# Kernel optimization log

Measured on AMD Instinct MI355X. Metric: run time of the kernel, lower is better.

## Reference

```python
import jax, jax.numpy as jnp
import numpy as np

H = 64        # index_n_heads
D = 128       # index_head_dim
R = 64        # rope_head_dim
TOPK = 512    # index_topk
FP8_MAX = 448.0
EPS = 1e-6
THETA = 10000.0


def setup_inputs() -> dict:
    key = jax.random.key(0)
    ks = jax.random.split(key, 6)
    T, DM, QL = 1536, 7168, 1536
    return {
        "hidden_states": jax.random.normal(ks[0], (T, DM), jnp.float32),
        "q_lora": jax.random.normal(ks[1], (T, QL), jnp.float32),
        "wq_b": jax.random.normal(ks[2], (QL, H * D), jnp.float32) / np.sqrt(QL),
        "wk": jax.random.normal(ks[3], (DM, D), jnp.float32) / np.sqrt(DM),
        "k_norm_w": jnp.ones((D,), jnp.float32),
        "k_norm_b": jnp.zeros((D,), jnp.float32),
        "weights_proj_w": jax.random.normal(ks[4], (DM, H), jnp.float32) / np.sqrt(DM),
        "positions": jnp.arange(T, dtype=jnp.int32),
    }


def _rope_neox(x, pos):
    # x: [T, ..., R]; pos: [T]. NEOX-style (half-split) rotary on the rope slice.
    half = R // 2
    inv = 1.0 / (THETA ** (jnp.arange(half, dtype=jnp.float32) / half))
    ang = pos.astype(jnp.float32)[:, None] * inv  # [T, half]
    cos, sin = jnp.cos(ang), jnp.sin(ang)
    while cos.ndim < x.ndim:
        cos, sin = cos[:, None, :], sin[:, None, :]
    x1, x2 = x[..., :half], x[..., half:]
    return jnp.concatenate([x1 * cos - x2 * sin, x2 * cos + x1 * sin], axis=-1)


def _fp8_quant(x):
    # per-row (last-dim) e4m3 quantization: value -> fp8 payload + fp32 scale
    scale = jnp.maximum(jnp.max(jnp.abs(x), axis=-1, keepdims=True) / FP8_MAX, 1e-12)
    xq = (x / scale).astype(jnp.float8_e4m3fn).astype(jnp.float32)
    return xq, scale


def reference(hidden_states, q_lora, wq_b, wk, k_norm_w, k_norm_b, weights_proj_w, positions):
    T = hidden_states.shape[0]
    softmax_scale = D ** (-0.5)
    weights_scale = H ** (-0.5)

    # projections
    q = (q_lora @ wq_b).reshape(T, H, D)          # wq_b
    k = hidden_states @ wk                        # wk

    # k_norm (LayerNorm)
    mu = jnp.mean(k, axis=-1, keepdims=True)
    var = jnp.mean((k - mu) ** 2, axis=-1, keepdims=True)
    k = (k - mu) * jax.lax.rsqrt(var + EPS) * k_norm_w + k_norm_b

    # RoPE on the first rope_head_dim dims of q and k
    q = jnp.concatenate([_rope_neox(q[..., :R], positions), q[..., R:]], axis=-1)
    k = jnp.concatenate([_rope_neox(k[..., :R], positions), k[..., R:]], axis=-1)

    # fp8 quantization (per token-head for q, per token for k)
    q_fp8, q_scale = _fp8_quant(q)   # [T,H,D], [T,H,1]
    k_fp8, k_scale = _fp8_quant(k)   # [T,D],   [T,1]

    # head-gate weights: weights_proj(x) * q_scale * softmax_scale * weights_scale
    gate = hidden_states @ weights_proj_w                      # [T,H]
    w = gate[..., None] * q_scale * (softmax_scale * weights_scale)  # [T,H,1]

    # index score: I[t,s] = sum_h w[t,h] * relu(q[t,h] . k[s]) * k_scale[s]
    qk = jnp.einsum('thd,sd->ths', q_fp8, k_fp8)               # [T,H,S]
    score = jnp.einsum('th,ths->ts', w[..., 0], jax.nn.relu(qk))
    score = score * k_scale[:, 0][None, :]

    # causal (ragged prefill) mask + topk block selection
    causal = positions[:, None] >= positions[None, :]
    score = jnp.where(causal, score, -jnp.inf)
    vals, idx = jax.lax.top_k(score, TOPK)
    idx = jnp.where(jnp.isfinite(vals), idx, -1)
    return idx, vals
```

## Files before the change

kernel.cpp:

```cpp
#include <hip/hip_runtime.h>
#include <hip/hip_bf16.h>
#include <math.h>

#define T_SZ 1536
#define DM_SZ 7168
#define QL_SZ 1536
#define H_SZ 64
#define D_SZ 128
#define ND 8192
#define TOPK_SZ 512
#define N2 192
#define SPLITK2 16

typedef float f32x4 __attribute__((ext_vector_type(4)));
typedef short s16x8 __attribute__((ext_vector_type(8)));
typedef unsigned long long u64;

static __device__ __forceinline__ unsigned char f32_to_e4m3(float x){
  unsigned int b = __float_as_uint(x);
  unsigned int s = (b >> 24) & 0x80u;
  float a = fabsf(x);
  if (a < 0.015625f){
    int m = (int)rintf(a * 512.0f);
    if (m == 8) return (unsigned char)(s | 0x08u);
    return (unsigned char)(s | (unsigned)m);
  }
  int e;
  float mant = frexpf(a, &e);
  int E = e - 1;
  int m = (int)rintf(mant * 16.0f) - 8;
  if (m == 8){ E += 1; m = 0; }
  if (E > 8 || (E == 8 && m > 6)) return (unsigned char)(s | 0x7Eu);
  return (unsigned char)(s | ((unsigned)(E + 7) << 3) | (unsigned)m);
}

static __device__ __forceinline__ unsigned short bf16_rne(float x){
  unsigned int u = __float_as_uint(x);
  return (unsigned short)((u + 0x7FFFu + ((u >> 16) & 1u)) >> 16);
}

typedef __attribute__((address_space(1))) const void gas_void;
typedef __attribute__((address_space(3))) void las_void;
static __device__ __forceinline__ void stage16(const void* g, void* l){
  __builtin_amdgcn_global_load_lds((gas_void*)g, (las_void*)l, 16, 0, 0);
}

__global__ void rope_table_k(const int* __restrict__ pos, float* __restrict__ cs){
  int i = blockIdx.x * blockDim.x + threadIdx.x;
  if (i >= T_SZ * 32) return;
  int t = i >> 5, j = i & 31;
  float inv = 1.0f / powf(10000.0f, (float)j * (1.0f / 32.0f));
  float ang = (float)pos[t] * inv;
  cs[t * 64 + j]      = cosf(ang);
  cs[t * 64 + 32 + j] = sinf(ang);
}

__global__ __launch_bounds__(256) void conv_split_k(const float* __restrict__ A,
                                                    unsigned short* __restrict__ hi,
                                                    unsigned short* __restrict__ lo,
                                                    int n4){
  int i = blockIdx.x * 256 + threadIdx.x;
  if (i >= n4) return;
  float4 v = *(const float4*)&A[(size_t)i * 4];
  float f[4] = {v.x, v.y, v.z, v.w};
  unsigned short hb[4], lb[4];
#pragma unroll
  for (int j = 0; j < 4; ++j){
    hb[j] = bf16_rne(f[j]);
    float hf = __uint_as_float((unsigned int)hb[j] << 16);
    lb[j] = bf16_rne(f[j] - hf);
  }
  ushort4 h, l;
  h.x = hb[0]; h.y = hb[1]; h.z = hb[2]; h.w = hb[3];
  l.x = lb[0]; l.y = lb[1]; l.z = lb[2]; l.w = lb[3];
  *(ushort4*)&hi[(size_t)i * 4] = h;
  *(ushort4*)&lo[(size_t)i * 4] = l;
}

__global__ __launch_bounds__(256) void convB_k(const float* __restrict__ B,
                                               unsigned short* __restrict__ bhi,
                                               unsigned short* __restrict__ blo){
  __shared__ float ld[32][33];
  const int n0 = blockIdx.x * 32, k0 = blockIdx.y * 32;
  const int t = threadIdx.x;
  const int r = t >> 3, c4 = (t & 7) * 4;
  float4 v = *(const float4*)&B[(size_t)(k0 + r) * ND + n0 + c4];
  ld[r][c4 + 0] = v.x; ld[r][c4 + 1] = v.y; ld[r][c4 + 2] = v.z; ld[r][c4 + 3] = v.w;
  __syncthreads();
  unsigned short hb[4], lb[4];
#pragma unroll
  for (int j = 0; j < 4; ++j){
    float x = ld[c4 + j][r];
    hb[j] = bf16_rne(x);
    float hf = __uint_as_float((unsigned int)hb[j] << 16);
    lb[j] = bf16_rne(x - hf);
  }
  ushort4 h, l;
  h.x = hb[0]; h.y = hb[1]; h.z = hb[2]; h.w = hb[3];
  l.x = lb[0]; l.y = lb[1]; l.z = lb[2]; l.w = lb[3];
  *(ushort4*)&bhi[(size_t)(n0 + r) * QL_SZ + k0 + c4] = h;
  *(ushort4*)&blo[(size_t)(n0 + r) * QL_SZ + k0 + c4] = l;
}

__global__ __launch_bounds__(256) void conv_w2_k(const float* __restrict__ wk,
                                                 const float* __restrict__ wp,
                                                 unsigned short* __restrict__ bhi,
                                                 unsigned short* __restrict__ blo){
  __shared__ float ld[32][33];
  const int n0 = blockIdx.x * 32, k0 = blockIdx.y * 32;
  const int t = threadIdx.x;
  const int r = t >> 3, c4 = (t & 7) * 4;
  float4 v;
  if (n0 < 128) v = *(const float4*)&wk[(size_t)(k0 + r) * 128 + n0 + c4];
  else          v = *(const float4*)&wp[(size_t)(k0 + r) * 64 + (n0 - 128) + c4];
  ld[r][c4 + 0] = v.x; ld[r][c4 + 1] = v.y; ld[r][c4 + 2] = v.z; ld[r][c4 + 3] = v.w;
  __syncthreads();
  unsigned short hb[4], lb[4];
#pragma unroll
  for (int j = 0; j < 4; ++j){
    float x = ld[c4 + j][r];
    hb[j] = bf16_rne(x);
    float hf = __uint_as_float((unsigned int)hb[j] << 16);
    lb[j] = bf16_rne(x - hf);
  }
  ushort4 h, l;
  h.x = hb[0]; h.y = hb[1]; h.z = hb[2]; h.w = hb[3];
  l.x = lb[0]; l.y = lb[1]; l.z = lb[2]; l.w = lb[3];
  *(ushort4*)&bhi[(size_t)(n0 + r) * DM_SZ + k0 + c4] = h;
  *(ushort4*)&blo[(size_t)(n0 + r) * DM_SZ + k0 + c4] = l;
}

__global__ __launch_bounds__(256) void gemm1_mfma_k(const unsigned short* __restrict__ Ahi,
                                                    const unsigned short* __restrict__ Alo,
                                                    const unsigned short* __restrict__ Bhi,
                                                    const unsigned short* __restrict__ Blo,
                                                    float* __restrict__ C){
  __shared__ unsigned short As [128 * 64];
  __shared__ unsigned short Bs0[128 * 64];
  __shared__ unsigned short Bs1[128 * 64];
  const int bid = blockIdx.x;
  const int lid = (bid & 7) * 96 + (bid >> 3);
  const int mt = lid % 12, nt = lid / 12;
  const int m0 = mt * 128, n0 = nt * 128;
  const int tid = threadIdx.x;
  const int w = tid >> 6, l = tid & 63;
  const int wr = w >> 1, wc = w & 1;
  const int lr = l & 15, lg = l >> 4;

  const int srow = w * 32 + (l >> 3);
  const int ssl  = (l & 7) ^ ((l >> 3) & 7);
  const size_t gA = (size_t)(m0 + srow) * QL_SZ + ssl * 8;
  const size_t gB = (size_t)(n0 + srow) * QL_SZ + ssl * 8;
  const int lbase = w * 2048;

  f32x4 acc[4][4];
#pragma unroll
  for (int i = 0; i < 4; ++i)
#pragma unroll
    for (int j = 0; j < 4; ++j) acc[i][j] = (f32x4){0.f, 0.f, 0.f, 0.f};

  const int amrow = wr * 64 + lr;
  const int bnrow = wc * 64 + lr;

  for (int k0 = 0; k0 < QL_SZ; k0 += 64){
#pragma unroll
    for (int i = 0; i < 4; ++i){
      size_t go = (size_t)i * 8 * QL_SZ + k0;
      stage16(Ahi + gA + go, As  + lbase + i * 512);
      stage16(Bhi + gB + go, Bs0 + lbase + i * 512);
      stage16(Blo + gB + go, Bs1 + lbase + i * 512);
    }
    __syncthreads();
#pragma unroll
    for (int kk = 0; kk < 2; ++kk){
      s16x8 af[4], b0[4], b1[4];
#pragma unroll
      for (int f = 0; f < 4; ++f){
        int ma = amrow + f * 16;
        int nb = bnrow + f * 16;
        int sa = ((kk * 4 + lg) ^ (ma & 7)) * 16;
        int sb = ((kk * 4 + lg) ^ (nb & 7)) * 16;
        af[f] = *(const s16x8*)((const char*)As  + ma * 128 + sa);
        b0[f] = *(const s16x8*)((const char*)Bs0 + nb * 128 + sb);
        b1[f] = *(const s16x8*)((const char*)Bs1 + nb * 128 + sb);
      }
#pragma unroll
      for (int fi = 0; fi < 4; ++fi)
#pragma unroll
        for (int fj = 0; fj < 4; ++fj)
          acc[fi][fj] = __builtin_amdgcn_mfma_f32_16x16x32_bf16(af[fi], b0[fj], acc[fi][fj], 0, 0, 0);
#pragma unroll
      for (int fi = 0; fi < 4; ++fi)
#pragma unroll
        for (int fj = 0; fj < 4; ++fj)
          acc[fi][fj] = __builtin_amdgcn_mfma_f32_16x16x32_bf16(af[fi], b1[fj], acc[fi][fj], 0, 0, 0);
    }
    __syncthreads();
#pragma unroll
    for (int i = 0; i < 4; ++i)
      stage16(Alo + gA + (size_t)i * 8 * QL_SZ + k0, As + lbase + i * 512);
    __syncthreads();
#pragma unroll
    for (int kk = 0; kk < 2; ++kk){
      s16x8 af[4], b0[4];
#pragma unroll
      for (int f = 0; f < 4; ++f){
        int ma = amrow + f * 16;
        int nb = bnrow + f * 16;
        af[f] = *(const s16x8*)((const char*)As  + ma * 128 + (((kk * 4 + lg) ^ (ma & 7)) * 16));
        b0[f] = *(const s16x8*)((const char*)Bs0 + nb * 128 + (((kk * 4 + lg) ^ (nb & 7)) * 16));
      }
#pragma unroll
      for (int fi = 0; fi < 4; ++fi)
#pragma unroll
        for (int fj = 0; fj < 4; ++fj)
          acc[fi][fj] = __builtin_amdgcn_mfma_f32_16x16x32_bf16(af[fi], b0[fj], acc[fi][fj], 0, 0, 0);
    }
    __syncthreads();
  }

#pragma unroll
  for (int fi = 0; fi < 4; ++fi){
    const int row = m0 + wr * 64 + fi * 16 + lg * 4;
#pragma unroll
    for (int fj = 0; fj < 4; ++fj){
      float* cp = C + (size_t)row * ND + n0 + wc * 64 + fj * 16 + lr;
      f32x4 d = acc[fi][fj];
      cp[0]              = d.x;
      cp[(size_t)ND]     = d.y;
      cp[(size_t)2 * ND] = d.z;
      cp[(size_t)3 * ND] = d.w;
    }
  }
}

__global__ __launch_bounds__(128) void gemm2_mfma_k(const unsigned short* __restrict__ Ahi,
                                                    const unsigned short* __restrict__ Alo,
                                                    const unsigned short* __restrict__ Bhi,
                                                    const unsigned short* __restrict__ Blo,
                                                    float* __restrict__ part){
  __shared__ unsigned short As [128 * 64];
  __shared__ unsigned short Bs0[64 * 64];
  __shared__ unsigned short Bs1[64 * 64];
  const int bid = blockIdx.x;
  const int lid = (bid & 7) * 72 + (bid >> 3);
  const int s   = lid / 36;
  const int rem = lid % 36;
  const int mt = rem / 3, nt = rem % 3;
  const int m0 = mt * 128, n0 = nt * 64;
  const int kbeg = s * (DM_SZ / SPLITK2);
  const int tid = threadIdx.x;
  const int w = tid >> 6, l = tid & 63;
  const int lr = l & 15, lg = l >> 4;

  const int srow = tid >> 3;
  const int ssl  = (tid & 7) ^ (srow & 7);
  const size_t gA = (size_t)(m0 + srow) * DM_SZ + ssl * 8;
  const size_t gB = (size_t)(n0 + srow) * DM_SZ + ssl * 8;
  const int lbase = w * 512;

  f32x4 acc[4][4];
#pragma unroll
  for (int i = 0; i < 4; ++i)
#pragma unroll
    for (int j = 0; j < 4; ++j) acc[i][j] = (f32x4){0.f, 0.f, 0.f, 0.f};

  const int amrow = w * 64 + lr;
  const int bnrow = lr;

  for (int k0 = kbeg; k0 < kbeg + DM_SZ / SPLITK2; k0 += 64){
#pragma unroll
    for (int i = 0; i < 8; ++i)
      stage16(Ahi + gA + (size_t)i * 16 * DM_SZ + k0, As + lbase + i * 1024);
#pragma unroll
    for (int i = 0; i < 4; ++i){
      stage16(Bhi + gB + (size_t)i * 16 * DM_SZ + k0, Bs0 + lbase + i * 1024);
      stage16(Blo + gB + (size_t)i * 16 * DM_SZ + k0, Bs1 + lbase + i * 1024);
    }
    __syncthreads();
#pragma unroll
    for (int kk = 0; kk < 2; ++kk){
      s16x8 af[4], b0[4], b1[4];
#pragma unroll
      for (int f = 0; f < 4; ++f){
        int ma = amrow + f * 16;
        int nb = bnrow + f * 16;
        int sa = ((kk * 4 + lg) ^ (ma & 7)) * 16;
        int sb = ((kk * 4 + lg) ^ (nb & 7)) * 16;
        af[f] = *(const s16x8*)((const char*)As  + ma * 128 + sa);
        b0[f] = *(const s16x8*)((const char*)Bs0 + nb * 128 + sb);
        b1[f] = *(const s16x8*)((const char*)Bs1 + nb * 128 + sb);
      }
#pragma unroll
      for (int fi = 0; fi < 4; ++fi)
#pragma unroll
        for (int fj = 0; fj < 4; ++fj)
          acc[fi][fj] = __builtin_amdgcn_mfma_f32_16x16x32_bf16(af[fi], b0[fj], acc[fi][fj], 0, 0, 0);
#pragma unroll
      for (int fi = 0; fi < 4; ++fi)
#pragma unroll
        for (int fj = 0; fj < 4; ++fj)
          acc[fi][fj] = __builtin_amdgcn_mfma_f32_16x16x32_bf16(af[fi], b1[fj], acc[fi][fj], 0, 0, 0);
    }
    __syncthreads();
#pragma unroll
    for (int i = 0; i < 8; ++i)
      stage16(Alo + gA + (size_t)i * 16 * DM_SZ + k0, As + lbase + i * 1024);
    __syncthreads();
#pragma unroll
    for (int kk = 0; kk < 2; ++kk){
      s16x8 af[4], b0[4];
#pragma unroll
      for (int f = 0; f < 4; ++f){
        int ma = amrow + f * 16;
        int nb = bnrow + f * 16;
        af[f] = *(const s16x8*)((const char*)As  + ma * 128 + (((kk * 4 + lg) ^ (ma & 7)) * 16));
        b0[f] = *(const s16x8*)((const char*)Bs0 + nb * 128 + (((kk * 4 + lg) ^ (nb & 7)) * 16));
      }
#pragma unroll
      for (int fi = 0; fi < 4; ++fi)
#pragma unroll
        for (int fj = 0; fj < 4; ++fj)
          acc[fi][fj] = __builtin_amdgcn_mfma_f32_16x16x32_bf16(af[fi], b0[fj], acc[fi][fj], 0, 0, 0);
    }
    __syncthreads();
  }

  float* p = part + (size_t)(s * 36 + mt * 3 + nt) * (128 * 64);
#pragma unroll
  for (int fi = 0; fi < 4; ++fi){
    const int row = w * 64 + fi * 16 + lg * 4;
#pragma unroll
    for (int fj = 0; fj < 4; ++fj){
      float* cp = p + (size_t)row * 64 + fj * 16 + lr;
      f32x4 d = acc[fi][fj];
      cp[  0] = d.x;
      cp[ 64] = d.y;
      cp[128] = d.z;
      cp[192] = d.w;
    }
  }
}

__global__ void gemm2_reduce2_k(const float* __restrict__ part,
                                float* __restrict__ kraw, float* __restrict__ gate){
  int e = blockIdx.x * 256 + threadIdx.x;
  if (e >= T_SZ * N2) return;
  int r = e / N2, c = e % N2;
  int mt = r >> 7, rl = r & 127;
  int nt = c >> 6, cl = c & 63;
  const float* pp = part + (size_t)(mt * 3 + nt) * (128 * 64) + rl * 64 + cl;
  float sum = 0.0f;
#pragma unroll
  for (int s = 0; s < SPLITK2; ++s) sum += pp[(size_t)s * 36 * 128 * 64];
  if (c < 128) kraw[r * 128 + c] = sum;
  else         gate[r * 64 + (c - 128)] = sum;
}

__global__ __launch_bounds__(256) void gemm1_k(const float* __restrict__ A,
                                               const float* __restrict__ B,
                                               float* __restrict__ C){
  __shared__ float As[8][132];
  __shared__ float Bs[8][132];
  const int tid = threadIdx.x;
  const int bm = blockIdx.y * 128, bn = blockIdx.x * 128;
  const int ty = tid >> 4, tx = tid & 15;
  const int arow = tid >> 1, ak = (tid & 1) * 4;
  const int brow = tid >> 5, bcol = (tid & 31) * 4;
  float acc[8][8];
#pragma unroll
  for (int i = 0; i < 8; i++)
#pragma unroll
    for (int j = 0; j < 8; j++) acc[i][j] = 0.0f;

  for (int k0 = 0; k0 < QL_SZ; k0 += 8){
    float4 av = *(const float4*)&A[(size_t)(bm + arow) * QL_SZ + k0 + ak];
    float4 bv = *(const float4*)&B[(size_t)(k0 + brow) * ND + bn + bcol];
    As[ak + 0][arow] = av.x; As[ak + 1][arow] = av.y;
    As[ak + 2][arow] = av.z; As[ak + 3][arow] = av.w;
    *(float4*)&Bs[brow][bcol] = bv;
    __syncthreads();
#pragma unroll
    for (int kk = 0; kk < 8; ++kk){
      float a[8], b[8];
      *(float4*)&a[0] = *(const float4*)&As[kk][ty * 8];
      *(float4*)&a[4] = *(const float4*)&As[kk][ty * 8 + 4];
      *(float4*)&b[0] = *(const float4*)&Bs[kk][tx * 8];
      *(float4*)&b[4] = *(const float4*)&Bs[kk][tx * 8 + 4];
#pragma unroll
      for (int i = 0; i < 8; i++)
#pragma unroll
        for (int j = 0; j < 8; j++) acc[i][j] += a[i] * b[j];
    }
    __syncthreads();
  }
#pragma unroll
  for (int i = 0; i < 8; i++)
#pragma unroll
    for (int j = 0; j < 8; j += 4){
      float4 o; o.x = acc[i][j]; o.y = acc[i][j+1]; o.z = acc[i][j+2]; o.w = acc[i][j+3];
      *(float4*)&C[(size_t)(bm + ty * 8 + i) * ND + bn + tx * 8 + j] = o;
    }
}

__global__ __launch_bounds__(256) void gemm2_partial_k(const float* __restrict__ hs,
                                                       const float* __restrict__ wk,
                                                       const float* __restrict__ wp,
                                                       float* __restrict__ part){
  __shared__ float As[32][33];
  __shared__ float Bs[32][196];
  const int tid = threadIdx.x;
  const int m0 = blockIdx.x * 32;
  const int ks = blockIdx.y;
  const int kbeg = ks * (DM_SZ / 8), kend = kbeg + DM_SZ / 8;
  const int arow = tid >> 3, ak4 = (tid & 7) * 4;
  const int r2 = (tid >> 4) * 2, cg = (tid & 15) * 12;
  float acc[2][12];
#pragma unroll
  for (int i = 0; i < 2; i++)
#pragma unroll
    for (int j = 0; j < 12; j++) acc[i][j] = 0.0f;

  for (int k0 = kbeg; k0 < kend; k0 += 32){
    float4 av = *(const float4*)&hs[(size_t)(m0 + arow) * DM_SZ + k0 + ak4];
    As[ak4 + 0][arow] = av.x; As[ak4 + 1][arow] = av.y;
    As[ak4 + 2][arow] = av.z; As[ak4 + 3][arow] = av.w;
#pragma unroll
    for (int i = 0; i < 6; ++i){
      int fi = tid + i * 256;
      int row = fi / 48, c4 = fi % 48;
      float4 bv;
      if (c4 < 32) bv = *(const float4*)&wk[(size_t)(k0 + row) * 128 + c4 * 4];
      else         bv = *(const float4*)&wp[(size_t)(k0 + row) * 64 + (c4 - 32) * 4];
      *(float4*)&Bs[row][c4 * 4] = bv;
    }
    __syncthreads();
#pragma unroll
    for (int kk = 0; kk < 32; ++kk){
      float a0 = As[kk][r2], a1 = As[kk][r2 + 1];
      float b[12];
      *(float4*)&b[0] = *(const float4*)&Bs[kk][cg];
      *(float4*)&b[4] = *(const float4*)&Bs[kk][cg + 4];
      *(float4*)&b[8] = *(const float4*)&Bs[kk][cg + 8];
#pragma unroll
      for (int j = 0; j < 12; j++){ acc[0][j] += a0 * b[j]; acc[1][j] += a1 * b[j]; }
    }
    __syncthreads();
  }
  float* p = part + (size_t)(ks * 48 + blockIdx.x) * 32 * 192;
#pragma unroll
  for (int i = 0; i < 2; i++)
#pragma unroll
    for (int j = 0; j < 12; j += 4){
      float4 o; o.x = acc[i][j]; o.y = acc[i][j+1]; o.z = acc[i][j+2]; o.w = acc[i][j+3];
      *(float4*)&p[(r2 + i) * 192 + cg + j] = o;
    }
}

__global__ void gemm2_reduce_k(const float* __restrict__ part,
                               float* __restrict__ kraw, float* __restrict__ gate){
  int e = blockIdx.x * 256 + threadIdx.x;
  if (e >= T_SZ * 192) return;
  int r = e / 192, c = e % 192;
  int mt = r >> 5, rl = r & 31;
  float s = 0.0f;
  for (int ks = 0; ks < 8; ++ks)
    s += part[((size_t)(ks * 48 + mt) * 32 + rl) * 192 + c];
  if (c < 128) kraw[r * 128 + c] = s;
  else         gate[r * 64 + (c - 128)] = s;
}

__global__ __launch_bounds__(128) void k_post_k(const float* __restrict__ kraw,
                                                const float* __restrict__ knw,
                                                const float* __restrict__ knb,
                                                const float* __restrict__ cs,
                                                unsigned char* __restrict__ kf8,
                                                float* __restrict__ kscale){
  const int t = blockIdx.x, d = threadIdx.x;
  __shared__ float sh[128];
  __shared__ float red[2];
  float x = kraw[t * 128 + d];
  float v = x;
#pragma unroll
  for (int o = 32; o > 0; o >>= 1) v += __shfl_xor(v, o, 64);
  if ((d & 63) == 0) red[d >> 6] = v;
  __syncthreads();
  float mu = (red[0] + red[1]) / 128.0f;
  float dx = x - mu;
  v = dx * dx;
  __syncthreads();
#pragma unroll
  for (int o = 32; o > 0; o >>= 1) v += __shfl_xor(v, o, 64);
  if ((d & 63) == 0) red[d >> 6] = v;
  __syncthreads();
  float var = (red[0] + red[1]) / 128.0f;
  float nv = dx * (1.0f / sqrtf(var + 1e-6f)) * knw[d] + knb[d];
  sh[d] = nv;
  __syncthreads();
  float outv;
  const float* ct = cs + t * 64;
  if (d < 32)        outv = nv * ct[d] - sh[d + 32] * ct[32 + d];
  else if (d < 64){ int j = d - 32; outv = nv * ct[j] + sh[j] * ct[32 + j]; }
  else               outv = nv;
  v = fabsf(outv);
  __syncthreads();
#pragma unroll
  for (int o = 32; o > 0; o >>= 1) v = fmaxf(v, __shfl_xor(v, o, 64));
  if ((d & 63) == 0) red[d >> 6] = v;
  __syncthreads();
  float amax = fmaxf(red[0], red[1]);
  float scale = fmaxf(amax / 448.0f, 1e-12f);
  kf8[t * 128 + d] = f32_to_e4m3(outv / scale);
  if (d == 0) kscale[t] = scale;
}

__global__ __launch_bounds__(256) void q_post2_k(const float* __restrict__ q,
                                                 const float* __restrict__ gate,
                                                 const float* __restrict__ cs,
                                                 unsigned char* __restrict__ qf8,
                                                 float* __restrict__ wbuf){
  const int t = blockIdx.x, tid = threadIdx.x;
  const int h = tid >> 2, g = tid & 3;
  __shared__ float sh[64 * 132];
  const float* qrow = q + (size_t)t * 8192;
#pragma unroll
  for (int i = 0; i < 8; ++i){
    int e4 = tid + i * 256;
    int hh = e4 >> 5, dd = (e4 & 31) * 4;
    float4 v = *(const float4*)&qrow[(size_t)e4 * 4];
    float* dst = &sh[hh * 132 + dd];
    dst[0] = v.x; dst[1] = v.y; dst[2] = v.z; dst[3] = v.w;
  }
  __syncthreads();
  const float* ct = cs + t * 64;
  const float* hq = sh + h * 132;
  float x[32];
#pragma unroll
  for (int j = 0; j < 32; ++j) x[j] = hq[g + 4 * j];
  float vals[32];
  float am = 0.0f;
#pragma unroll
  for (int j = 0; j < 8; ++j){
    int d = g + 4 * j;
    float c = ct[d], s = ct[32 + d];
    float lo = x[j] * c - x[j + 8] * s;
    float hi = x[j + 8] * c + x[j] * s;
    vals[j] = lo; vals[j + 8] = hi;
    am = fmaxf(am, fmaxf(fabsf(lo), fabsf(hi)));
  }
#pragma unroll
  for (int j = 16; j < 32; ++j){ vals[j] = x[j]; am = fmaxf(am, fabsf(x[j])); }
  am = fmaxf(am, __shfl_xor(am, 1, 64));
  am = fmaxf(am, __shfl_xor(am, 2, 64));
  float scale = fmaxf(am / 448.0f, 1e-12f);
  unsigned char* qp = qf8 + (size_t)t * 8192 + h * 128 + g;
#pragma unroll
  for (int j = 0; j < 32; ++j) qp[4 * j] = f32_to_e4m3(vals[j] / scale);
  if (g == 0) wbuf[t * 64 + h] = gate[t * 64 + h] * scale * 0.011048543456039806f;
}

__global__ __launch_bounds__(256) void score_mfma_k(const unsigned char* __restrict__ qf8,
                                                    const unsigned char* __restrict__ kf8,
                                                    const float* __restrict__ wbuf,
                                                    const float* __restrict__ kscale,
                                                    float* __restrict__ score){
  const int bid = blockIdx.x;
  const int p = bid >> 1;
  const int h0 = (bid & 1) * 32;
  int bt = (int)((sqrtf(8.0f * (float)p + 1.0f) - 1.0f) * 0.5f);
  while ((bt + 1) * (bt + 2) / 2 <= p) ++bt;
  while (bt * (bt + 1) / 2 > p) --bt;
  const int bs = p - bt * (bt + 1) / 2;
  const int t0 = bt * 64, s0 = bs * 64;
  const int tid = threadIdx.x;
  const int w  = tid >> 6;
  const int l  = tid & 63;
  const int lr = l & 15;
  const int lg = l >> 4;

  __shared__ float wl[64][68];
#pragma unroll
  for (int i = 0; i < 4; i++){
    int fi = tid + i * 256;
    int row = fi >> 4, c4 = (fi & 15) * 4;
    *(float4*)&wl[row][c4] = *(const float4*)&wbuf[(t0 + row) * 64 + c4];
  }

  u64 b00,b01,b02,b03, b10,b11,b12,b13, b20,b21,b22,b23, b30,b31,b32,b33;
  {
    const unsigned char* kb = kf8 + (size_t)s0 * 128 + 8 * lg;
    const unsigned char* k0r = kb + (size_t)(lr     ) * 128;
    const unsigned char* k1r = kb + (size_t)(lr + 16) * 128;
    const unsigned char* k2r = kb + (size_t)(lr + 32) * 128;
    const unsigned char* k3r = kb + (size_t)(lr + 48) * 128;
    b00=*(const u64*)(k0r+0);  b01=*(const u64*)(k0r+32); b02=*(const u64*)(k0r+64); b03=*(const u64*)(k0r+96);
    b10=*(const u64*)(k1r+0);  b11=*(const u64*)(k1r+32); b12=*(const u64*)(k1r+64); b13=*(const u64*)(k1r+96);
    b20=*(const u64*)(k2r+0);  b21=*(const u64*)(k2r+32); b22=*(const u64*)(k2r+64); b23=*(const u64*)(k2r+96);
    b30=*(const u64*)(k3r+0);  b31=*(const u64*)(k3r+32); b32=*(const u64*)(k3r+64); b33=*(const u64*)(k3r+96);
  }
  __syncthreads();

  const unsigned char* qp = qf8 + (size_t)(t0 + 16 * w + lr) * 8192 + h0 * 128 + 8 * lg;
  u64 a0 = *(const u64*)(qp +  0), a1 = *(const u64*)(qp + 32),
      a2 = *(const u64*)(qp + 64), a3 = *(const u64*)(qp + 96);

  f32x4 acc0 = {0,0,0,0}, acc1 = {0,0,0,0}, acc2 = {0,0,0,0}, acc3 = {0,0,0,0};
  const int wrow = 16 * w + 4 * lg;

  for (int h = 0; h < 32; ++h){
    const unsigned char* qn = qp + ((h + 1) & 31) * 128;
    u64 p0 = *(const u64*)(qn +  0), p1 = *(const u64*)(qn + 32),
        p2 = *(const u64*)(qn + 64), p3 = *(const u64*)(qn + 96);

    f32x4 c0 = {0,0,0,0}, c1 = {0,0,0,0}, c2 = {0,0,0,0}, c3 = {0,0,0,0};
    c0 = __builtin_amdgcn_mfma_f32_16x16x32_fp8_fp8((long)a0, (long)b00, c0, 0, 0, 0);
    c1 = __builtin_amdgcn_mfma_f32_16x16x32_fp8_fp8((long)a0, (long)b10, c1, 0, 0, 0);
    c2 = __builtin_amdgcn_mfma_f32_16x16x32_fp8_fp8((long)a0, (long)b20, c2, 0, 0, 0);
    c3 = __builtin_amdgcn_mfma_f32_16x16x32_fp8_fp8((long)a0, (long)b30, c3, 0, 0, 0);
    c0 = __builtin_amdgcn_mfma_f32_16x16x32_fp8_fp8((long)a1, (long)b01, c0, 0, 0, 0);
    c1 = __builtin_amdgcn_mfma_f32_16x16x32_fp8_fp8((long)a1, (long)b11, c1, 0, 0, 0);
    c2 = __builtin_amdgcn_mfma_f32_16x16x32_fp8_fp8((long)a1, (long)b21, c2, 0, 0, 0);
    c3 = __builtin_amdgcn_mfma_f32_16x16x32_fp8_fp8((long)a1, (long)b31, c3, 0, 0, 0);
    c0 = __builtin_amdgcn_mfma_f32_16x16x32_fp8_fp8((long)a2, (long)b02, c0, 0, 0, 0);
    c1 = __builtin_amdgcn_mfma_f32_16x16x32_fp8_fp8((long)a2, (long)b12, c1, 0, 0, 0);
    c2 = __builtin_amdgcn_mfma_f32_16x16x32_fp8_fp8((long)a2, (long)b22, c2, 0, 0, 0);
    c3 = __builtin_amdgcn_mfma_f32_16x16x32_fp8_fp8((long)a2, (long)b32, c3, 0, 0, 0);
    c0 = __builtin_amdgcn_mfma_f32_16x16x32_fp8_fp8((long)a3, (long)b03, c0, 0, 0, 0);
    c1 = __builtin_amdgcn_mfma_f32_16x16x32_fp8_fp8((long)a3, (long)b13, c1, 0, 0, 0);
    c2 = __builtin_amdgcn_mfma_f32_16x16x32_fp8_fp8((long)a3, (long)b23, c2, 0, 0, 0);
    c3 = __builtin_amdgcn_mfma_f32_16x16x32_fp8_fp8((long)a3, (long)b33, c3, 0, 0, 0);

    float w0 = wl[wrow + 0][h0 + h], w1 = wl[wrow + 1][h0 + h],
          w2 = wl[wrow + 2][h0 + h], w3 = wl[wrow + 3][h0 + h];
    acc0.x += w0 * fmaxf(c0.x, 0.0f); acc0.y += w1 * fmaxf(c0.y, 0.0f);
    acc0.z += w2 * fmaxf(c0.z, 0.0f); acc0.w += w3 * fmaxf(c0.w, 0.0f);
    acc1.x += w0 * fmaxf(c1.x, 0.0f); acc1.y += w1 * fmaxf(c1.y, 0.0f);
    acc1.z += w2 * fmaxf(c1.z, 0.0f); acc1.w += w3 * fmaxf(c1.w, 0.0f);
    acc2.x += w0 * fmaxf(c2.x, 0.0f); acc2.y += w1 * fmaxf(c2.y, 0.0f);
    acc2.z += w2 * fmaxf(c2.z, 0.0f); acc2.w += w3 * fmaxf(c2.w, 0.0f);
    acc3.x += w0 * fmaxf(c3.x, 0.0f); acc3.y += w1 * fmaxf(c3.y, 0.0f);
    acc3.z += w2 * fmaxf(c3.z, 0.0f); acc3.w += w3 * fmaxf(c3.w, 0.0f);

    a0 = p0; a1 = p1; a2 = p2; a3 = p3;
  }

  const int trow = t0 + 16 * w + 4 * lg;
  float ks0 = kscale[s0 + lr], ks1 = kscale[s0 + 16 + lr],
        ks2 = kscale[s0 + 32 + lr], ks3 = kscale[s0 + 48 + lr];
  float* sbase = score + (size_t)(bid & 1) * T_SZ * T_SZ;
  float* sp0 = sbase + (size_t)(trow + 0) * T_SZ + s0 + lr;
  float* sp1 = sbase + (size_t)(trow + 1) * T_SZ + s0 + lr;
  float* sp2 = sbase + (size_t)(trow + 2) * T_SZ + s0 + lr;
  float* sp3 = sbase + (size_t)(trow + 3) * T_SZ + s0 + lr;
  sp0[ 0] = acc0.x * ks0; sp1[ 0] = acc0.y * ks0; sp2[ 0] = acc0.z * ks0; sp3[ 0] = acc0.w * ks0;
  sp0[16] = acc1.x * ks1; sp1[16] = acc1.y * ks1; sp2[16] = acc1.z * ks1; sp3[16] = acc1.w * ks1;
  sp0[32] = acc2.x * ks2; sp1[32] = acc2.y * ks2; sp2[32] = acc2.z * ks2; sp3[32] = acc2.w * ks2;
  sp0[48] = acc3.x * ks3; sp1[48] = acc3.y * ks3; sp2[48] = acc3.z * ks3; sp3[48] = acc3.w * ks3;
}

__global__ __launch_bounds__(256) void topk_sel_k(const float* __restrict__ score,
                                                  float* __restrict__ out){
  const int t = blockIdx.x, tid = threadIdx.x;
  const int n = t + 1;
  __shared__ unsigned int U[2048];
  __shared__ unsigned long long cand[512];
  __shared__ unsigned int hist[256];
  __shared__ unsigned int tix[1536];
  __shared__ unsigned int cnts[2];
  __shared__ unsigned int sel[2];

  const float* s0row = score + (size_t)t * T_SZ;
  const float* s1row = score + (size_t)T_SZ * T_SZ + (size_t)t * T_SZ;
#pragma unroll
  for (int m = 0; m < 8; ++m){
    int j = tid + m * 256;
    unsigned int u = 0u;
    if (j < n){
      float val = s0row[j] + s1row[j];
      unsigned int b = __float_as_uint(val);
      u = (b & 0x80000000u) ? ~b : (b | 0x80000000u);
    }
    U[j] = u;
  }
  if (tid < 2) cnts[tid] = 0u;
  __syncthreads();

  if (n > 512){
    unsigned int prefix = 0u, rem = 512u;
#pragma unroll
    for (int level = 0; level < 4; ++level){
      const int shift = 24 - 8 * level;
      hist[tid] = 0u;
      __syncthreads();
#pragma unroll
      for (int m = 0; m < 8; ++m){
        unsigned int u = U[tid + m * 256];
        bool match = (u != 0u) && (level == 0 || (u >> (shift + 8)) == prefix);
        if (match) atomicAdd(&hist[(u >> shift) & 255u], 1u);
      }
      __syncthreads();
      if (tid < 64){
        unsigned int c0 = hist[tid*4], c1 = hist[tid*4+1], c2 = hist[tid*4+2], c3 = hist[tid*4+3];
        unsigned int loc = c0 + c1 + c2 + c3;
        unsigned int acc = loc;
        for (int off = 1; off < 64; off <<= 1){
          unsigned int v = __shfl_down(acc, off, 64);
          if (tid + off < 64) acc += v;
        }
        unsigned int S3 = acc - loc;
        unsigned int S2 = S3 + c3;
        unsigned int S1 = S2 + c2;
        unsigned int S0 = S1 + c1;
        if (S0 < rem && rem <= S0 + c0){ sel[0] = tid*4 + 0; sel[1] = S0; }
        if (S1 < rem && rem <= S1 + c1){ sel[0] = tid*4 + 1; sel[1] = S1; }
        if (S2 < rem && rem <= S2 + c2){ sel[0] = tid*4 + 2; sel[1] = S2; }
        if (S3 < rem && rem <= S3 + c3){ sel[0] = tid*4 + 3; sel[1] = S3; }
      }
      __syncthreads();
      prefix = (prefix << 8) | sel[0];
      rem -= sel[1];
    }
    const unsigned int u_thr = prefix;

#pragma unroll
    for (int m = 0; m < 8; ++m){
      int j = tid + m * 256;
      unsigned int u = U[j];
      if (u > u_thr){
        unsigned int p = atomicAdd(&cnts[0], 1u);
        cand[p] = ((unsigned long long)u << 32) | (unsigned int)(~(unsigned int)j);
      } else if (u == u_thr){
        unsigned int q = atomicAdd(&cnts[1], 1u);
        tix[q] = (unsigned int)j;
      }
    }
    __syncthreads();
    const unsigned int G = cnts[0], Tt = cnts[1];
    if (Tt == rem){
      for (unsigned int q = tid; q < Tt; q += 256)
        cand[G + q] = ((unsigned long long)u_thr << 32) | (unsigned int)(~tix[q]);
      __syncthreads();
    } else {
      if (tid < 64) hist[tid] = 0u;
      __syncthreads();
      for (unsigned int q = tid; q < Tt; q += 256) atomicAdd(&hist[tix[q] >> 5], 1u);
      __syncthreads();
      if (tid == 0){
        unsigned int cum = 0; unsigned int d = 0;
        for (; d < 64; ++d){ unsigned int c = hist[d]; if (cum + c >= rem) break; cum += c; }
        sel[0] = d; sel[1] = rem - cum;
      }
      __syncthreads();
      const unsigned int dA = sel[0], remA = sel[1];
      if (tid < 32) hist[64 + tid] = 0u;
      __syncthreads();
      for (unsigned int q = tid; q < Tt; q += 256){
        unsigned int j = tix[q];
        if ((j >> 5) == dA) atomicAdd(&hist[64 + (j & 31u)], 1u);
      }
      __syncthreads();
      if (tid == 0){
        unsigned int cum = 0; unsigned int e = 0;
        for (; e < 32; ++e){ unsigned int c = hist[64 + e]; if (cum + c >= remA) break; cum += c; }
        sel[0] = dA * 32 + e;
        cnts[1] = 0u;
      }
      __syncthreads();
      const unsigned int jthr = sel[0];
      for (unsigned int q = tid; q < Tt; q += 256){
        unsigned int j = tix[q];
        if (j <= jthr){
          unsigned int p = atomicAdd(&cnts[1], 1u);
          cand[G + p] = ((unsigned long long)u_thr << 32) | (unsigned int)(~j);
        }
      }
      __syncthreads();
    }
  } else {
    for (int i = tid; i < 512; i += 256){
      unsigned int u = (i < n) ? U[i] : 0u;
      cand[i] = u ? (((unsigned long long)u << 32) | (unsigned int)(~(unsigned int)i)) : 0ull;
    }
    __syncthreads();
  }

  u64 a = cand[2 * tid], b = cand[2 * tid + 1];
#pragma unroll
  for (int k = 2; k <= 512; k <<= 1){
#pragma unroll
    for (int j = k >> 1; j >= 1; j >>= 1){
      if (j >= 128){
        __syncthreads();
        cand[2 * tid] = a; cand[2 * tid + 1] = b;
        __syncthreads();
        int e0 = 2 * tid;
        u64 p0 = cand[e0 ^ j], p1 = cand[(e0 + 1) ^ j];
        bool up  = ((e0 & k) == 0);
        bool low = ((e0 & j) == 0);
        bool mx = (up == low);
        a = mx ? (a > p0 ? a : p0) : (a < p0 ? a : p0);
        b = mx ? (b > p1 ? b : p1) : (b < p1 ? b : p1);
      } else if (j >= 2){
        int d = j >> 1;
        u64 p0 = __shfl_xor(a, d, 64);
        u64 p1 = __shfl_xor(b, d, 64);
        bool up  = (((2 * tid) & k) == 0);
        bool low = ((tid & d) == 0);
        bool mx = (up == low);
        a = mx ? (a > p0 ? a : p0) : (a < p0 ? a : p0);
        b = mx ? (b > p1 ? b : p1) : (b < p1 ? b : p1);
      } else {
        bool up = (((2 * tid) & k) == 0);
        u64 mn = a < b ? a : b, mxv = a < b ? b : a;
        a = up ? mxv : mn;
        b = up ? mn : mxv;
      }
    }
  }

#pragma unroll
  for (int m = 0; m < 2; ++m){
    int i = 2 * tid + m;
    u64 kk = m ? b : a;
    unsigned int u = (unsigned int)(kk >> 32);
    unsigned int bb = (u & 0x80000000u) ? (u & 0x7fffffffu) : ~u;
    float val = __uint_as_float(bb);
    int idx = (int)(~(unsigned int)(kk & 0xffffffffu));
    bool fin = (u != 0u) && (val > -__builtin_huge_valf());
    out[(size_t)t * TOPK_SZ + i] = fin ? (float)idx : -1.0f;
    out[(size_t)T_SZ * TOPK_SZ + (size_t)t * TOPK_SZ + i] = fin ? val : -3.0e38f;
  }
}

extern "C" void kernel_launch(void* const* d_in, const int* in_sizes, int n_in,
                              void* d_out, int out_size, void* d_ws, size_t ws_size,
                              hipStream_t stream){
  const float* hs  = (const float*)d_in[0];
  const float* ql  = (const float*)d_in[1];
  const float* wqb = (const float*)d_in[2];
  const float* wk  = (const float*)d_in[3];
  const float* knw = (const float*)d_in[4];
  const float* knb = (const float*)d_in[5];
  const float* wpj = (const float*)d_in[6];
  const int*   pos = (const int*)d_in[7];
  char* ws = (char*)d_ws;
  size_t off = 0;
  auto alloc = [&](size_t b){ size_t o = off; off += (b + 255) & ~(size_t)255; return o; };
  float* cs     = (float*)(ws + alloc((size_t)T_SZ * 64 * 4));
  float* qbuf   = (float*)(ws + alloc((size_t)T_SZ * ND * 4));
  float* kraw   = (float*)(ws + alloc((size_t)T_SZ * 128 * 4));
  float* gate   = (float*)(ws + alloc((size_t)T_SZ * 64 * 4));
  unsigned char* kf8 = (unsigned char*)(ws + alloc((size_t)T_SZ * 128));
  float* kscale = (float*)(ws + alloc((size_t)T_SZ * 4));
  float* wbuf   = (float*)(ws + alloc((size_t)T_SZ * 64 * 4));
  const size_t base2 = off;

  size_t oA = base2;
  auto allocA = [&](size_t b){ size_t o = oA; oA += (b + 255) & ~(size_t)255; return o; };
  unsigned short* hshi = (unsigned short*)(ws + allocA((size_t)T_SZ * DM_SZ * 2));
  unsigned short* hslo = (unsigned short*)(ws + allocA((size_t)T_SZ * DM_SZ * 2));
  unsigned short* w2hi = (unsigned short*)(ws + allocA((size_t)N2 * DM_SZ * 2));
  unsigned short* w2lo = (unsigned short*)(ws + allocA((size_t)N2 * DM_SZ * 2));
  float* part2 = (float*)(ws + allocA((size_t)SPLITK2 * 36 * 128 * 64 * 4));
  const bool fitA = (oA <= ws_size);

  size_t oB = base2;
  auto allocB = [&](size_t b){ size_t o = oB; oB += (b + 255) & ~(size_t)255; return o; };
  unsigned short* Ahi = (unsigned short*)(ws + allocB((size_t)T_SZ * QL_SZ * 2));
  unsigned short* Alo = (unsigned short*)(ws + allocB((size_t)T_SZ * QL_SZ * 2));
  unsigned short* Bth = (unsigned short*)(ws + allocB((size_t)ND * QL_SZ * 2));
  unsigned short* Btl = (unsigned short*)(ws + allocB((size_t)ND * QL_SZ * 2));
  const bool fitB = (oB <= ws_size);

  unsigned char* qf8 = (unsigned char*)(ws + base2);
  float* part_old    = (float*)(ws + base2);
  float* score = qbuf;
  float* out = (float*)d_out;

  rope_table_k<<<dim3((T_SZ * 32 + 255) / 256), dim3(256), 0, stream>>>(pos, cs);

  if (fitA){
    conv_split_k<<<dim3(T_SZ * DM_SZ / 4 / 256), dim3(256), 0, stream>>>(hs, hshi, hslo, T_SZ * DM_SZ / 4);
    conv_w2_k<<<dim3(N2 / 32, DM_SZ / 32), dim3(256), 0, stream>>>(wk, wpj, w2hi, w2lo);
    gemm2_mfma_k<<<dim3(12 * 3 * SPLITK2), dim3(128), 0, stream>>>(hshi, hslo, w2hi, w2lo, part2);
    gemm2_reduce2_k<<<dim3((T_SZ * N2 + 255) / 256), dim3(256), 0, stream>>>(part2, kraw, gate);
  } else {
    gemm2_partial_k<<<dim3(48, 8), dim3(256), 0, stream>>>(hs, wk, wpj, part_old);
    gemm2_reduce_k<<<dim3((T_SZ * 192) / 256), dim3(256), 0, stream>>>(part_old, kraw, gate);
  }
  k_post_k<<<dim3(T_SZ), dim3(128), 0, stream>>>(kraw, knw, knb, cs, kf8, kscale);

  if (fitB){
    conv_split_k<<<dim3(T_SZ * QL_SZ / 4 / 256), dim3(256), 0, stream>>>(ql, Ahi, Alo, T_SZ * QL_SZ / 4);
    convB_k<<<dim3(ND / 32, QL_SZ / 32), dim3(256), 0, stream>>>(wqb, Bth, Btl);
    gemm1_mfma_k<<<dim3(768), dim3(256), 0, stream>>>(Ahi, Alo, Bth, Btl, qbuf);
  } else {
    gemm1_k<<<dim3(ND / 128, T_SZ / 128), dim3(256), 0, stream>>>(ql, wqb, qbuf);
  }
  q_post2_k<<<dim3(T_SZ), dim3(256), 0, stream>>>(qbuf, gate, cs, qf8, wbuf);

  score_mfma_k<<<dim3(600), dim3(256), 0, stream>>>(qf8, kf8, wbuf, kscale, score);
  topk_sel_k<<<dim3(T_SZ), dim3(256), 0, stream>>>(score, out);
}
```

Measured before the change: 269.6 us.

## Fuse hidden-state bf16 split into gemm2 and stage A hi/lo together

In gemm2 the separate conv_split_k pass over hidden_states is removed. The kernel now loads fp32 hidden_states directly, splits each value into bf16 hi/lo parts in registers, and writes both to swizzled LDS. Both GEMMs now stage A-hi and A-lo into separate LDS buffers at the same time, so the second sync-and-restage phase per k-step goes away. This saves a full write and re-read of the large split activation arrays and two barriers per iteration. In exchange it uses more LDS and registers, adds conversion ALU work inside the GEMM, and redoes the conversion for each N-tile that reads the same A rows.

```diff
diff --git a/kernel.cpp b/kernel.cpp
--- a/kernel.cpp
+++ b/kernel.cpp
@@ -135,7 +135,8 @@
                                                     const unsigned short* __restrict__ Bhi,
                                                     const unsigned short* __restrict__ Blo,
                                                     float* __restrict__ C){
-  __shared__ unsigned short As [128 * 64];
+  __shared__ unsigned short As0[128 * 64];
+  __shared__ unsigned short As1[128 * 64];
   __shared__ unsigned short Bs0[128 * 64];
   __shared__ unsigned short Bs1[128 * 64];
   const int bid = blockIdx.x;
@@ -166,21 +167,23 @@
 #pragma unroll
     for (int i = 0; i < 4; ++i){
       size_t go = (size_t)i * 8 * QL_SZ + k0;
-      stage16(Ahi + gA + go, As  + lbase + i * 512);
+      stage16(Ahi + gA + go, As0 + lbase + i * 512);
+      stage16(Alo + gA + go, As1 + lbase + i * 512);
       stage16(Bhi + gB + go, Bs0 + lbase + i * 512);
       stage16(Blo + gB + go, Bs1 + lbase + i * 512);
     }
     __syncthreads();
 #pragma unroll
     for (int kk = 0; kk < 2; ++kk){
-      s16x8 af[4], b0[4], b1[4];
+      s16x8 ah[4], al[4], b0[4], b1[4];
 #pragma unroll
       for (int f = 0; f < 4; ++f){
         int ma = amrow + f * 16;
         int nb = bnrow + f * 16;
         int sa = ((kk * 4 + lg) ^ (ma & 7)) * 16;
         int sb = ((kk * 4 + lg) ^ (nb & 7)) * 16;
-        af[f] = *(const s16x8*)((const char*)As  + ma * 128 + sa);
+        ah[f] = *(const s16x8*)((const char*)As0 + ma * 128 + sa);
+        al[f] = *(const s16x8*)((const char*)As1 + ma * 128 + sa);
         b0[f] = *(const s16x8*)((const char*)Bs0 + nb * 128 + sb);
         b1[f] = *(const s16x8*)((const char*)Bs1 + nb * 128 + sb);
       }
@@ -188,33 +191,17 @@
       for (int fi = 0; fi < 4; ++fi)
 #pragma unroll
         for (int fj = 0; fj < 4; ++fj)
-          acc[fi][fj] = __builtin_amdgcn_mfma_f32_16x16x32_bf16(af[fi], b0[fj], acc[fi][fj], 0, 0, 0);
+          acc[fi][fj] = __builtin_amdgcn_mfma_f32_16x16x32_bf16(ah[fi], b0[fj], acc[fi][fj], 0, 0, 0);
 #pragma unroll
       for (int fi = 0; fi < 4; ++fi)
 #pragma unroll
         for (int fj = 0; fj < 4; ++fj)
-          acc[fi][fj] = __builtin_amdgcn_mfma_f32_16x16x32_bf16(af[fi], b1[fj], acc[fi][fj], 0, 0, 0);
-    }
-    __syncthreads();
-#pragma unroll
-    for (int i = 0; i < 4; ++i)
-      stage16(Alo + gA + (size_t)i * 8 * QL_SZ + k0, As + lbase + i * 512);
-    __syncthreads();
-#pragma unroll
-    for (int kk = 0; kk < 2; ++kk){
-      s16x8 af[4], b0[4];
-#pragma unroll
-      for (int f = 0; f < 4; ++f){
-        int ma = amrow + f * 16;
-        int nb = bnrow + f * 16;
-        af[f] = *(const s16x8*)((const char*)As  + ma * 128 + (((kk * 4 + lg) ^ (ma & 7)) * 16));
-        b0[f] = *(const s16x8*)((const char*)Bs0 + nb * 128 + (((kk * 4 + lg) ^ (nb & 7)) * 16));
-      }
+          acc[fi][fj] = __builtin_amdgcn_mfma_f32_16x16x32_bf16(ah[fi], b1[fj], acc[fi][fj], 0, 0, 0);
 #pragma unroll
       for (int fi = 0; fi < 4; ++fi)
 #pragma unroll
         for (int fj = 0; fj < 4; ++fj)
-          acc[fi][fj] = __builtin_amdgcn_mfma_f32_16x16x32_bf16(af[fi], b0[fj], acc[fi][fj], 0, 0, 0);
+          acc[fi][fj] = __builtin_amdgcn_mfma_f32_16x16x32_bf16(al[fi], b0[fj], acc[fi][fj], 0, 0, 0);
     }
     __syncthreads();
   }
@@ -234,12 +221,12 @@
   }
 }
 
-__global__ __launch_bounds__(128) void gemm2_mfma_k(const unsigned short* __restrict__ Ahi,
-                                                    const unsigned short* __restrict__ Alo,
+__global__ __launch_bounds__(128) void gemm2_mfma_k(const float* __restrict__ hs,
                                                     const unsigned short* __restrict__ Bhi,
                                                     const unsigned short* __restrict__ Blo,
                                                     float* __restrict__ part){
-  __shared__ unsigned short As [128 * 64];
+  __shared__ unsigned short As0[128 * 64];
+  __shared__ unsigned short As1[128 * 64];
   __shared__ unsigned short Bs0[64 * 64];
   __shared__ unsigned short Bs1[64 * 64];
   const int bid = blockIdx.x;
@@ -255,7 +242,6 @@
 
   const int srow = tid >> 3;
   const int ssl  = (tid & 7) ^ (srow & 7);
-  const size_t gA = (size_t)(m0 + srow) * DM_SZ + ssl * 8;
   const size_t gB = (size_t)(n0 + srow) * DM_SZ + ssl * 8;
   const int lbase = w * 512;
 
@@ -269,25 +255,50 @@
   const int bnrow = lr;
 
   for (int k0 = kbeg; k0 < kbeg + DM_SZ / SPLITK2; k0 += 64){
-#pragma unroll
-    for (int i = 0; i < 8; ++i)
-      stage16(Ahi + gA + (size_t)i * 16 * DM_SZ + k0, As + lbase + i * 1024);
+    f32x4 av[16];
+#pragma unroll
+    for (int i = 0; i < 8; ++i){
+      int idx8 = tid + i * 128;
+      int ar = idx8 >> 3, as = idx8 & 7;
+      const float* src = hs + (size_t)(m0 + ar) * DM_SZ + k0 + as * 8;
+      av[2 * i]     = *(const f32x4*)src;
+      av[2 * i + 1] = *(const f32x4*)(src + 4);
+    }
 #pragma unroll
     for (int i = 0; i < 4; ++i){
       stage16(Bhi + gB + (size_t)i * 16 * DM_SZ + k0, Bs0 + lbase + i * 1024);
       stage16(Blo + gB + (size_t)i * 16 * DM_SZ + k0, Bs1 + lbase + i * 1024);
     }
+#pragma unroll
+    for (int i = 0; i < 8; ++i){
+      int idx8 = tid + i * 128;
+      int ar = idx8 >> 3, as = idx8 & 7;
+      float f[8];
+      *(f32x4*)&f[0] = av[2 * i];
+      *(f32x4*)&f[4] = av[2 * i + 1];
+      unsigned short hb[8], lb[8];
+#pragma unroll
+      for (int j = 0; j < 8; ++j){
+        hb[j] = bf16_rne(f[j]);
+        float hf = __uint_as_float((unsigned int)hb[j] << 16);
+        lb[j] = bf16_rne(f[j] - hf);
+      }
+      int loff = ar * 64 + (as ^ (ar & 7)) * 8;
+      *(s16x8*)&As0[loff] = *(s16x8*)hb;
+      *(s16x8*)&As1[loff] = *(s16x8*)lb;
+    }
     __syncthreads();
 #pragma unroll
     for (int kk = 0; kk < 2; ++kk){
-      s16x8 af[4], b0[4], b1[4];
+      s16x8 ah[4], al[4], b0[4], b1[4];
 #pragma unroll
       for (int f = 0; f < 4; ++f){
         int ma = amrow + f * 16;
         int nb = bnrow + f * 16;
         int sa = ((kk * 4 + lg) ^ (ma & 7)) * 16;
         int sb = ((kk * 4 + lg) ^ (nb & 7)) * 16;
-        af[f] = *(const s16x8*)((const char*)As  + ma * 128 + sa);
+        ah[f] = *(const s16x8*)((const char*)As0 + ma * 128 + sa);
+        al[f] = *(const s16x8*)((const char*)As1 + ma * 128 + sa);
         b0[f] = *(const s16x8*)((const char*)Bs0 + nb * 128 + sb);
         b1[f] = *(const s16x8*)((const char*)Bs1 + nb * 128 + sb);
       }
@@ -295,33 +306,17 @@
       for (int fi = 0; fi < 4; ++fi)
 #pragma unroll
         for (int fj = 0; fj < 4; ++fj)
-          acc[fi][fj] = __builtin_amdgcn_mfma_f32_16x16x32_bf16(af[fi], b0[fj], acc[fi][fj], 0, 0, 0);
+          acc[fi][fj] = __builtin_amdgcn_mfma_f32_16x16x32_bf16(ah[fi], b0[fj], acc[fi][fj], 0, 0, 0);
 #pragma unroll
       for (int fi = 0; fi < 4; ++fi)
 #pragma unroll
         for (int fj = 0; fj < 4; ++fj)
-          acc[fi][fj] = __builtin_amdgcn_mfma_f32_16x16x32_bf16(af[fi], b1[fj], acc[fi][fj], 0, 0, 0);
-    }
-    __syncthreads();
-#pragma unroll
-    for (int i = 0; i < 8; ++i)
-      stage16(Alo + gA + (size_t)i * 16 * DM_SZ + k0, As + lbase + i * 1024);
-    __syncthreads();
-#pragma unroll
-    for (int kk = 0; kk < 2; ++kk){
-      s16x8 af[4], b0[4];
-#pragma unroll
-      for (int f = 0; f < 4; ++f){
-        int ma = amrow + f * 16;
-        int nb = bnrow + f * 16;
-        af[f] = *(const s16x8*)((const char*)As  + ma * 128 + (((kk * 4 + lg) ^ (ma & 7)) * 16));
-        b0[f] = *(const s16x8*)((const char*)Bs0 + nb * 128 + (((kk * 4 + lg) ^ (nb & 7)) * 16));
-      }
+          acc[fi][fj] = __builtin_amdgcn_mfma_f32_16x16x32_bf16(ah[fi], b1[fj], acc[fi][fj], 0, 0, 0);
 #pragma unroll
       for (int fi = 0; fi < 4; ++fi)
 #pragma unroll
         for (int fj = 0; fj < 4; ++fj)
-          acc[fi][fj] = __builtin_amdgcn_mfma_f32_16x16x32_bf16(af[fi], b0[fj], acc[fi][fj], 0, 0, 0);
+          acc[fi][fj] = __builtin_amdgcn_mfma_f32_16x16x32_bf16(al[fi], b0[fj], acc[fi][fj], 0, 0, 0);
     }
     __syncthreads();
   }
@@ -857,8 +852,6 @@
 
   size_t oA = base2;
   auto allocA = [&](size_t b){ size_t o = oA; oA += (b + 255) & ~(size_t)255; return o; };
-  unsigned short* hshi = (unsigned short*)(ws + allocA((size_t)T_SZ * DM_SZ * 2));
-  unsigned short* hslo = (unsigned short*)(ws + allocA((size_t)T_SZ * DM_SZ * 2));
   unsigned short* w2hi = (unsigned short*)(ws + allocA((size_t)N2 * DM_SZ * 2));
   unsigned short* w2lo = (unsigned short*)(ws + allocA((size_t)N2 * DM_SZ * 2));
   float* part2 = (float*)(ws + allocA((size_t)SPLITK2 * 36 * 128 * 64 * 4));
@@ -880,9 +873,8 @@
   rope_table_k<<<dim3((T_SZ * 32 + 255) / 256), dim3(256), 0, stream>>>(pos, cs);
 
   if (fitA){
-    conv_split_k<<<dim3(T_SZ * DM_SZ / 4 / 256), dim3(256), 0, stream>>>(hs, hshi, hslo, T_SZ * DM_SZ / 4);
     conv_w2_k<<<dim3(N2 / 32, DM_SZ / 32), dim3(256), 0, stream>>>(wk, wpj, w2hi, w2lo);
-    gemm2_mfma_k<<<dim3(12 * 3 * SPLITK2), dim3(128), 0, stream>>>(hshi, hslo, w2hi, w2lo, part2);
+    gemm2_mfma_k<<<dim3(12 * 3 * SPLITK2), dim3(128), 0, stream>>>(hs, w2hi, w2lo, part2);
     gemm2_reduce2_k<<<dim3((T_SZ * N2 + 255) / 256), dim3(256), 0, stream>>>(part2, kraw, gate);
   } else {
     gemm2_partial_k<<<dim3(48, 8), dim3(256), 0, stream>>>(hs, wk, wpj, part_old);
```

Result: slower. 276.7 us (+2.7%).
